# Kernel optimization log

Measured on AMD Instinct MI355X. Metric: run time of the kernel, lower is better.

The kernel has to match this reference:

```python
import jax, jax.numpy as jnp
import numpy as np

SEQ_LEN = 4096
NUM_EIGH = 40
D_IN = 64
D_OUT = 64
K_U = 3
BSZ = 2


def _spectral_filters(L, K):
    # Hankel matrix Z_ij = 2/((i+j)^3 - (i+j)), i,j in [1, L]
    e = np.arange(1, L + 1, dtype=np.float64)
    s = e[:, None] + e[None, :]
    Z = 2.0 / (s ** 3 - s)
    sigma, phi = np.linalg.eigh(Z)
    phi_k = phi[:, -K:] * sigma[-K:] ** 0.25  # (L, K)
    return jnp.asarray(phi_k, dtype=jnp.float32)


def setup_inputs() -> dict:
    key = jax.random.key(0)
    kx, km, kp, kn = jax.random.split(key, 4)
    x = jax.random.normal(kx, (BSZ, SEQ_LEN, D_IN), dtype=jnp.float32)
    phi = _spectral_filters(SEQ_LEN, NUM_EIGH)  # (L, K)
    M = jax.random.normal(km, (D_OUT, D_IN, K_U), dtype=jnp.float32) / D_IN
    M_phi_plus = jax.random.normal(kp, (NUM_EIGH, D_IN, D_OUT), dtype=jnp.float32) / 10.0
    M_phi_minus = jax.random.normal(kn, (NUM_EIGH, D_IN, D_OUT), dtype=jnp.float32) / 10.0
    return {"x": x, "phi": phi, "M": M, "M_phi_plus": M_phi_plus, "M_phi_minus": M_phi_minus}


def _stu_forward(x, phi, M, M_phi_plus, M_phi_minus):
    bsz, L, d_in = x.shape
    n = int(2 ** np.ceil(np.log2(2 * L - 1)))  # FFT length (8192)
    t = jnp.arange(L)
    sgn = jnp.where(t % 2 == 1, -1.0, 1.0).astype(x.dtype)  # (L,)

    # FFT of [u, u*sgn] once over d_in (K-expansion deferred to freq domain; FFT is linear)
    U = jnp.stack([x, x * sgn[None, :, None]], axis=-1)        # (b, L, d, 2)
    U_f = jnp.fft.rfft(U, n=n, axis=1)                         # (b, nf, d, 2)
    v_f = jnp.fft.rfft(phi.astype(jnp.float32), n=n, axis=0)   # (nf, K)

    prod = v_f[None, :, :, None, None] * U_f[:, :, None, :, :]  # (b, nf, K, d, 2)
    U_conv = jnp.fft.irfft(prod, n=n, axis=1)[:, :L]            # (b, L, K, d, 2)
    U_plus = U_conv[..., 0]
    U_minus = U_conv[..., 1] * sgn[None, :, None, None]

    # spectral tensordot: contract (K, d_in) -> d_out
    spec = (jnp.einsum('blkd,kdo->blo', U_plus, M_phi_plus)
            + jnp.einsum('blkd,kdo->blo', U_minus, M_phi_minus))

    ar = jnp.zeros((bsz, L, M.shape[0]), dtype=x.dtype)
    for i in range(M.shape[2]):  # k_u is small and fixed
        y_i = jnp.einsum('bli,oi->blo', x, M[:, :, i])
        if i > 0:
            y_i = jnp.pad(y_i[:, : L - i], ((0, 0), (i, 0), (0, 0)))
        ar = ar + y_i
    return spec + ar


def reference(x, phi, M, M_phi_plus, M_phi_minus):
    return _stu_forward(x, phi, M, M_phi_plus, M_phi_minus)
```

## Files before the change

### kernel.cpp

```cpp
#include <hip/hip_runtime.h>

typedef short bf16x8 __attribute__((ext_vector_type(8)));
typedef float f32x4 __attribute__((ext_vector_type(4)));
typedef unsigned short u16;

__device__ __forceinline__ u16 f2bf(float f) {
    unsigned u = __builtin_bit_cast(unsigned, f);
    return (u16)((u + 0x7fffu + ((u >> 16) & 1u)) >> 16);
}

__global__ __launch_bounds__(256)
void k_pre(const float* __restrict__ Mp, const float* __restrict__ Mm,
           float* __restrict__ ApT, float* __restrict__ AmT,
           float* __restrict__ out, int* __restrict__ counter) {
    __shared__ float tp[64 * 65], tm[64 * 65];
    if (blockIdx.x < 40) {
        const int k = blockIdx.x, tid = threadIdx.x;
        for (int f = tid; f < 4096; f += 256) {
            int d = f >> 6, o = f & 63;
            float p = Mp[k * 4096 + f], m = Mm[k * 4096 + f];
            tp[o * 65 + d] = p + m;
            tm[o * 65 + d] = p - m;
        }
        __syncthreads();
        for (int f = tid; f < 4096; f += 256) {
            int o = f >> 6, d = f & 63;
            ApT[k * 4096 + f] = tp[o * 65 + d];
            AmT[k * 4096 + f] = tm[o * 65 + d];
        }
    } else {
        const int bz = blockIdx.x - 40;
        if (bz == 0 && threadIdx.x == 0) *counter = 0;
        float* po = out + bz * 4096;
        #pragma unroll
        for (int i = 0; i < 4; ++i)
            *(f32x4*)(po + (threadIdx.x + i * 256) * 4) = (f32x4){0.f, 0.f, 0.f, 0.f};
    }
}

__global__ __launch_bounds__(256)
void k_mid(const float* __restrict__ x, u16* __restrict__ xpad,
           const float* __restrict__ phi, const float* __restrict__ ApT,
           const float* __restrict__ AmT, const float* __restrict__ Mar,
           u16* __restrict__ wg) {
    if (blockIdx.x < 256) {
        const int u = blockIdx.x;
        #pragma unroll
        for (int i = 0; i < 4; ++i) {
            int gid = (u * 4 + i) * 256 + threadIdx.x;
            int b = gid >> 17, rem = gid & 131071;
            int r = rem >> 4, c4 = rem & 15;
            u16 o0 = 0, o1 = 0, o2 = 0, o3 = 0;
            if (r >= 4096) {
                const f32x4 v = *(const f32x4*)(x + ((b << 12) + (r - 4096)) * 64 + c4 * 4);
                o0 = f2bf(v.x); o1 = f2bf(v.y); o2 = f2bf(v.z); o3 = f2bf(v.w);
            }
            u16* p = xpad + ((b << 13) + r) * 64 + c4 * 4;
            p[0] = o0; p[1] = o1; p[2] = o2; p[3] = o3;
        }
    } else {
        const int bi  = blockIdx.x - 256;
        const int par = bi & 1;
        const int sbq = bi >> 1;
        const int sb  = sbq >> 4, qb = sbq & 15;
        const int q   = qb * 256 + threadIdx.x;
        const int o   = q >> 6, d = q & 63;
        const float* A = (par ? AmT : ApT);

        const int nt_  = o >> 4, m15_ = o & 15;
        const int ks_  = d >> 5, q4_ = (d >> 3) & 3, e_ = d & 7;
        const int pidx = ((ks_ * 4 + nt_) * 64 + (q4_ * 16 + m15_)) * 8 + e_;

        float a[40];
        #pragma unroll
        for (int k = 0; k < 40; ++k) a[k] = A[k * 4096 + q];

        #pragma unroll 2
        for (int m = 0; m < 32; ++m) {
            const int s = sb * 64 + 2 * m + par;
            const float* ph = phi + s * 40;
            float e0 = 0.f, e1 = 0.f;
            #pragma unroll
            for (int k = 0; k < 40; k += 2) { e0 += ph[k] * a[k]; e1 += ph[k + 1] * a[k + 1]; }
            float ev = e0 + e1;
            if (s < 3) ev += Mar[o * 192 + d * 3 + s];
            wg[(size_t)s * 4096 + pidx] = f2bf(ev);
        }
    }
}

__global__ __launch_bounds__(256, 2)
void k_spectral(const u16* __restrict__ xpad, const u16* __restrict__ wg,
                float* __restrict__ out, int* __restrict__ counter) {
    __shared__ __align__(16) u16 xs[2 * 191 * 64];
    __shared__ int sh;

    const int tid  = threadIdx.x;
    const int lane = tid & 63, w = tid >> 6;
    const int m15  = lane & 15, q4 = lane >> 4;
    const int th   = w >> 1, batch = w & 1;

    for (;;) {
        __syncthreads();
        if (tid == 0) sh = atomicAdd(counter, 1);
        __syncthreads();
        const int U = sh;
        if (U >= 1120) break;

        int mu = U, shalf = 0, slen = 64;
        if (U >= 992) { mu = 992 + ((U - 992) >> 1); shalf = (U - 992) & 1; slen = 32; }
        int g = 0;
        #pragma unroll 1
        while (g < 31 && (g + 1) * (64 - g) <= mu) ++g;
        const int rem = mu - g * (65 - g);
        const int cnt = 32 - g;
        const int col = (rem >= cnt) ? 1 : 0;
        const int J = 2 * g + col;
        const int I = g + (col ? rem - cnt : rem);
        const int t0 = I << 7, s0 = (J << 6) + (shalf << 5);
        const int nrows = 127 + slen;
        const int base = 4096 + t0 - s0 - (slen - 1);

        #pragma unroll
        for (int b = 0; b < 2; ++b) {
            #pragma unroll 1
            for (int f = tid; f < nrows * 8; f += 256) {
                int r = f >> 3, c = f & 7;
                bf16x8 v = *(const bf16x8*)(xpad + (size_t)((b << 13) + base + r) * 64 + c * 8);
                *(bf16x8*)(xs + ((b * 191 + r) * 8 + (c ^ (r & 7))) * 8) = v;
            }
        }
        __syncthreads();

        f32x4 acc[4][4];
        #pragma unroll
        for (int mt = 0; mt < 4; ++mt)
            #pragma unroll
            for (int nt = 0; nt < 4; ++nt)
                acc[mt][nt] = (f32x4){0.f, 0.f, 0.f, 0.f};

        const u16* xb = xs + batch * (191 * 64);
        const int rb = th * 64 + (slen - 1) + m15;

#define LOADW(BUF, S)                                                          \
        {                                                                      \
            const u16* wp_ = wg + (size_t)(S) * 4096 + lane * 8;               \
            _Pragma("unroll")                                                  \
            for (int f = 0; f < 8; ++f) BUF[f] = *(const bf16x8*)(wp_ + f * 512); \
        }

#define COMPUTE_S(BUF, DS)                                                     \
        {                                                                      \
            const int ds_ = (DS);                                              \
            _Pragma("unroll")                                                  \
            for (int ks = 0; ks < 2; ++ks) {                                   \
                const int kq = ks * 4 + q4;                                    \
                _Pragma("unroll")                                              \
                for (int mt = 0; mt < 4; ++mt) {                               \
                    int r = rb + mt * 16 - ds_;                                \
                    bf16x8 av = *(const bf16x8*)(xb + (r * 8 + (kq ^ (r & 7))) * 8); \
                    acc[mt][0] = __builtin_amdgcn_mfma_f32_16x16x32_bf16(av, BUF[ks * 4 + 0], acc[mt][0], 0, 0, 0); \
                    acc[mt][1] = __builtin_amdgcn_mfma_f32_16x16x32_bf16(av, BUF[ks * 4 + 1], acc[mt][1], 0, 0, 0); \
                    acc[mt][2] = __builtin_amdgcn_mfma_f32_16x16x32_bf16(av, BUF[ks * 4 + 2], acc[mt][2], 0, 0, 0); \
                    acc[mt][3] = __builtin_amdgcn_mfma_f32_16x16x32_bf16(av, BUF[ks * 4 + 3], acc[mt][3], 0, 0, 0); \
                }                                                              \
            }                                                                  \
        }

        bf16x8 b0[8], b1[8], b2[8], b3[8];
        const int half = slen >> 1;
        LOADW(b0, s0);     LOADW(b1, s0 + 1);
        LOADW(b2, s0 + 2); LOADW(b3, s0 + 3);
        #pragma unroll 1
        for (int j2 = 0; j2 < half; j2 += 2) {
            __builtin_amdgcn_s_setprio(1);
            COMPUTE_S(b0, 2 * j2);
            COMPUTE_S(b1, 2 * j2 + 1);
            __builtin_amdgcn_s_setprio(0);
            if (j2 + 2 < half) { LOADW(b0, s0 + 2 * j2 + 4); LOADW(b1, s0 + 2 * j2 + 5); }
            __builtin_amdgcn_s_setprio(1);
            COMPUTE_S(b2, 2 * j2 + 2);
            COMPUTE_S(b3, 2 * j2 + 3);
            __builtin_amdgcn_s_setprio(0);
            if (j2 + 2 < half) { LOADW(b2, s0 + 2 * j2 + 6); LOADW(b3, s0 + 2 * j2 + 7); }
        }
#undef LOADW
#undef COMPUTE_S

        #pragma unroll
        for (int mt = 0; mt < 4; ++mt) {
            int t = t0 + th * 64 + mt * 16 + q4 * 4;
            #pragma unroll
            for (int nt = 0; nt < 4; ++nt) {
                int o = nt * 16 + m15;
                float* op = out + (size_t)((batch << 12) + t) * 64 + o;
                #pragma unroll
                for (int r = 0; r < 4; ++r)
                    atomicAdd(op + r * 64, acc[mt][nt][r]);
            }
        }
    }
}

extern "C" void kernel_launch(void* const* d_in, const int* in_sizes, int n_in,
                              void* d_out, int out_size, void* d_ws, size_t ws_size,
                              hipStream_t stream) {
    const float* x   = (const float*)d_in[0];
    const float* phi = (const float*)d_in[1];
    const float* M   = (const float*)d_in[2];
    const float* Mp  = (const float*)d_in[3];
    const float* Mm  = (const float*)d_in[4];
    float* out = (float*)d_out;

    int* counter = (int*)d_ws;
    u16* xpad = (u16*)((char*)d_ws + 4096);
    u16* wg   = (u16*)((char*)d_ws + 4096 + 2097152);
    float* ApT = (float*)((char*)d_ws + 4096 + 2097152 + 33554432);
    float* AmT = ApT + 40 * 4096;

    k_pre<<<168, 256, 0, stream>>>(Mp, Mm, ApT, AmT, out, counter);
    k_mid<<<2304, 256, 0, stream>>>(x, xpad, phi, ApT, AmT, M, wg);
    k_spectral<<<512, 256, 0, stream>>>(xpad, wg, out, counter);
}
```

Before: 223.1 us.

## Fold M_phi combine into weight-generation kernel and drop the pre-pass launch

Removes the separate k_pre kernel: the sum and difference of M_phi_plus and M_phi_minus are now computed in registers inside k_mid, and the output zeroing and counter reset move into extra blocks of k_mid. Each weight-generation block now handles both parities over 128 time steps instead of one parity over 64, and the dot product uses four accumulators. This saves one kernel launch and the ApT/AmT round trip through global memory. In exchange there are fewer blocks (896 vs 2304), more registers per thread (80 floats held live), and the index mapping changes so that d comes from the high bits and o from the low bits of q.

```diff
diff --git a/kernel.cpp b/kernel.cpp
--- a/kernel.cpp
+++ b/kernel.cpp
@@ -10,41 +10,56 @@
 }
 
 __global__ __launch_bounds__(256)
-void k_pre(const float* __restrict__ Mp, const float* __restrict__ Mm,
-           float* __restrict__ ApT, float* __restrict__ AmT,
-           float* __restrict__ out, int* __restrict__ counter) {
-    __shared__ float tp[64 * 65], tm[64 * 65];
-    if (blockIdx.x < 40) {
-        const int k = blockIdx.x, tid = threadIdx.x;
-        for (int f = tid; f < 4096; f += 256) {
-            int d = f >> 6, o = f & 63;
-            float p = Mp[k * 4096 + f], m = Mm[k * 4096 + f];
-            tp[o * 65 + d] = p + m;
-            tm[o * 65 + d] = p - m;
-        }
-        __syncthreads();
-        for (int f = tid; f < 4096; f += 256) {
-            int o = f >> 6, d = f & 63;
-            ApT[k * 4096 + f] = tp[o * 65 + d];
-            AmT[k * 4096 + f] = tm[o * 65 + d];
-        }
-    } else {
-        const int bz = blockIdx.x - 40;
-        if (bz == 0 && threadIdx.x == 0) *counter = 0;
-        float* po = out + bz * 4096;
-        #pragma unroll
-        for (int i = 0; i < 4; ++i)
-            *(f32x4*)(po + (threadIdx.x + i * 256) * 4) = (f32x4){0.f, 0.f, 0.f, 0.f};
-    }
-}
-
-__global__ __launch_bounds__(256)
 void k_mid(const float* __restrict__ x, u16* __restrict__ xpad,
-           const float* __restrict__ phi, const float* __restrict__ ApT,
-           const float* __restrict__ AmT, const float* __restrict__ Mar,
-           u16* __restrict__ wg) {
-    if (blockIdx.x < 256) {
-        const int u = blockIdx.x;
+           const float* __restrict__ phi, const float* __restrict__ Mp,
+           const float* __restrict__ Mm, const float* __restrict__ Mar,
+           u16* __restrict__ wg, float* __restrict__ out,
+           int* __restrict__ counter) {
+    const int bi = blockIdx.x;
+    if (bi < 512) {
+        const int sb = bi >> 4, qb = bi & 15;
+        const int q  = qb * 256 + threadIdx.x;
+        const int d  = q >> 6, o = q & 63;
+
+        const int nt_  = o >> 4, m15_ = o & 15;
+        const int ks_  = d >> 5, q4_ = (d >> 3) & 3, e_ = d & 7;
+        const int pidx = ((ks_ * 4 + nt_) * 64 + (q4_ * 16 + m15_)) * 8 + e_;
+
+        float ap[40], am[40];
+        #pragma unroll
+        for (int k = 0; k < 40; ++k) {
+            float p = Mp[k * 4096 + q], m = Mm[k * 4096 + q];
+            ap[k] = p + m;
+            am[k] = p - m;
+        }
+
+        #pragma unroll 2
+        for (int m = 0; m < 64; ++m) {
+            #pragma unroll
+            for (int par = 0; par < 2; ++par) {
+                const int s = sb * 128 + 2 * m + par;
+                const float* ph = phi + s * 40;
+                float e0 = 0.f, e1 = 0.f, e2 = 0.f, e3 = 0.f;
+                if (par == 0) {
+                    #pragma unroll
+                    for (int k = 0; k < 40; k += 4) {
+                        e0 += ph[k] * ap[k];     e1 += ph[k + 1] * ap[k + 1];
+                        e2 += ph[k + 2] * ap[k + 2]; e3 += ph[k + 3] * ap[k + 3];
+                    }
+                } else {
+                    #pragma unroll
+                    for (int k = 0; k < 40; k += 4) {
+                        e0 += ph[k] * am[k];     e1 += ph[k + 1] * am[k + 1];
+                        e2 += ph[k + 2] * am[k + 2]; e3 += ph[k + 3] * am[k + 3];
+                    }
+                }
+                float ev = (e0 + e1) + (e2 + e3);
+                if (s < 3) ev += Mar[o * 192 + d * 3 + s];
+                wg[(size_t)s * 4096 + pidx] = f2bf(ev);
+            }
+        }
+    } else if (bi < 768) {
+        const int u = bi - 512;
         #pragma unroll
         for (int i = 0; i < 4; ++i) {
             int gid = (u * 4 + i) * 256 + threadIdx.x;
@@ -59,33 +74,12 @@
             p[0] = o0; p[1] = o1; p[2] = o2; p[3] = o3;
         }
     } else {
-        const int bi  = blockIdx.x - 256;
-        const int par = bi & 1;
-        const int sbq = bi >> 1;
-        const int sb  = sbq >> 4, qb = sbq & 15;
-        const int q   = qb * 256 + threadIdx.x;
-        const int o   = q >> 6, d = q & 63;
-        const float* A = (par ? AmT : ApT);
-
-        const int nt_  = o >> 4, m15_ = o & 15;
-        const int ks_  = d >> 5, q4_ = (d >> 3) & 3, e_ = d & 7;
-        const int pidx = ((ks_ * 4 + nt_) * 64 + (q4_ * 16 + m15_)) * 8 + e_;
-
-        float a[40];
-        #pragma unroll
-        for (int k = 0; k < 40; ++k) a[k] = A[k * 4096 + q];
-
-        #pragma unroll 2
-        for (int m = 0; m < 32; ++m) {
-            const int s = sb * 64 + 2 * m + par;
-            const float* ph = phi + s * 40;
-            float e0 = 0.f, e1 = 0.f;
-            #pragma unroll
-            for (int k = 0; k < 40; k += 2) { e0 += ph[k] * a[k]; e1 += ph[k + 1] * a[k + 1]; }
-            float ev = e0 + e1;
-            if (s < 3) ev += Mar[o * 192 + d * 3 + s];
-            wg[(size_t)s * 4096 + pidx] = f2bf(ev);
-        }
+        const int bz = bi - 768;
+        if (bz == 0 && threadIdx.x == 0) *counter = 0;
+        float* po = out + bz * 4096;
+        #pragma unroll
+        for (int i = 0; i < 4; ++i)
+            *(f32x4*)(po + (threadIdx.x + i * 256) * 4) = (f32x4){0.f, 0.f, 0.f, 0.f};
     }
 }
 
@@ -215,10 +209,7 @@
     int* counter = (int*)d_ws;
     u16* xpad = (u16*)((char*)d_ws + 4096);
     u16* wg   = (u16*)((char*)d_ws + 4096 + 2097152);
-    float* ApT = (float*)((char*)d_ws + 4096 + 2097152 + 33554432);
-    float* AmT = ApT + 40 * 4096;
-
-    k_pre<<<168, 256, 0, stream>>>(Mp, Mm, ApT, AmT, out, counter);
-    k_mid<<<2304, 256, 0, stream>>>(x, xpad, phi, ApT, AmT, M, wg);
+
+    k_mid<<<896, 256, 0, stream>>>(x, xpad, phi, Mp, Mm, M, wg, out, counter);
     k_spectral<<<512, 256, 0, stream>>>(xpad, wg, out, counter);
 }
```

Measured after the change: 290.3 us. 1.3x slower.
